# Optimization experiments

Hardware: AMD Instinct MI355X
Metric: run time of the kernel (lower is better)

## Reference

```python
import jax, jax.numpy as jnp
import numpy as np

Nh = 128
B = 4096


def _conv3d(x, w):
    # x: [B, C, D, H, W], w: [O, I, 3, 3, 3], same padding, no bias
    return jax.lax.conv_general_dilated(
        x, w, window_strides=(1, 1, 1), padding=[(1, 1)] * 3,
        dimension_numbers=("NCDHW", "OIDHW", "NCDHW"))


def setup_inputs() -> dict:
    key = jax.random.key(0)
    ks = jax.random.split(key, 12)
    x = jax.random.normal(ks[0], (B, 1024), dtype=jnp.float32)
    hidden_states = jax.random.normal(ks[1], (B, Nh, 4, 4, 4), dtype=jnp.float32)
    cw = 0.05  # small init for conv kernels
    Wz = jax.random.normal(ks[2], (Nh, Nh, 3, 3, 3), dtype=jnp.float32) * cw
    Wr = jax.random.normal(ks[3], (Nh, Nh, 3, 3, 3), dtype=jnp.float32) * cw
    Wm = jax.random.normal(ks[4], (Nh, Nh, 3, 3, 3), dtype=jnp.float32) * cw
    # biases init like np.random.rand -> uniform [0,1)
    bz = jax.random.uniform(ks[5], (1, Nh, 4, 4, 4), dtype=jnp.float32)
    br = jax.random.uniform(ks[6], (1, Nh, 4, 4, 4), dtype=jnp.float32)
    bm = jax.random.uniform(ks[7], (1, Nh, 4, 4, 4), dtype=jnp.float32)
    lw = 0.03
    Lz = jax.random.normal(ks[8], (Nh * 64, 1024), dtype=jnp.float32) * lw
    Lr = jax.random.normal(ks[9], (Nh * 64, 1024), dtype=jnp.float32) * lw
    Lm = jax.random.normal(ks[10], (Nh * 64, 1024), dtype=jnp.float32) * lw
    return dict(x=x, hidden_states=hidden_states, Wz=Wz, Wr=Wr, Wm=Wm,
                bz=bz, br=br, bm=bm, Lz=Lz, Lr=Lr, Lm=Lm)


def reference(x, hidden_states, Wz, Wr, Wm, bz, br, bm, Lz, Lr, Lm):
    # linear projections (torch Linear: x @ W.T), reshaped to voxel grid
    lz = (x @ Lz.T).reshape(B, Nh, 4, 4, 4)
    lr = (x @ Lr.T).reshape(B, Nh, 4, 4, 4)
    lm = (x @ Lm.T).reshape(B, Nh, 4, 4, 4)
    z = jax.nn.sigmoid(_conv3d(hidden_states, Wz) + lz + bz)
    r = jax.nn.sigmoid(_conv3d(hidden_states, Wr) + lr + br)
    mem = jnp.tanh(_conv3d(r * hidden_states, Wm) + lm + bm)
    return (1.0 - z) * hidden_states + z * mem
```

## Files before the change

kernel.cpp:

```cpp
#include <hip/hip_runtime.h>
#include <cstdint>

typedef __attribute__((ext_vector_type(8))) short bf16x8;
typedef __attribute__((ext_vector_type(4))) float f32x4;
typedef unsigned short u16;
typedef unsigned int u32;

static const size_t OFF_WT = 0;
static const size_t OFF_XB = 2654464;
static const size_t OFF_LB = 11043072;
static const size_t OFF_HT = 61374720;
static const size_t OFF_RH = 128483584;

__device__ __forceinline__ u16 f2bf(float x) {
  union { float f; u32 u; } v; v.f = x;
  u32 r = (v.u + 0x7FFFu + ((v.u >> 16) & 1u)) >> 16;
  return (u16)r;
}
__device__ __forceinline__ float bf2f(u16 x) {
  union { u32 u; float f; } v; v.u = ((u32)x) << 16; return v.f;
}

__device__ __forceinline__ void gload16(const void* g, void* l) {
  __builtin_amdgcn_global_load_lds(
      (const __attribute__((address_space(1))) uint32_t*)g,
      (__attribute__((address_space(3))) uint32_t*)l, 16, 0, 0);
}

__global__ __launch_bounds__(256) void k_cvt(
    const float* __restrict__ x,
    const float* __restrict__ Wz, const float* __restrict__ Wr, const float* __restrict__ Wm,
    const float* __restrict__ Lz, const float* __restrict__ Lr, const float* __restrict__ Lm,
    uint8_t* __restrict__ ws) {
  u16* wt = (u16*)(ws + OFF_WT);
  u16* xb = (u16*)(ws + OFF_XB);
  u16* lb = (u16*)(ws + OFF_LB);
  const long NWT = 3L * 27 * 128 * 128;
  const long NX  = 4096L * 1024;
  const long NL  = 3L * 8192 * 1024;
  const long total = NWT + NX + NL;
  for (long i = (long)blockIdx.x * blockDim.x + threadIdx.x; i < total;
       i += (long)gridDim.x * blockDim.x) {
    if (i < NWT) {
      long g = i / (27L * 16384);
      long r = i % (27L * 16384);
      long t = r / 16384;
      long oc = (r / 128) % 128;
      long ic = r % 128;
      const float* W = (g == 0) ? Wz : ((g == 1) ? Wr : Wm);
      wt[i] = f2bf(W[(oc * 128 + ic) * 27 + t]);
    } else if (i < NWT + NX) {
      long j = i - NWT;
      xb[j] = f2bf(x[j]);
    } else {
      long j = i - NWT - NX;
      long g = j / (8192L * 1024);
      long r = j % (8192L * 1024);
      const float* L = (g == 0) ? Lz : ((g == 1) ? Lr : Lm);
      lb[j] = f2bf(L[r]);
    }
  }
}

__global__ __launch_bounds__(256) void k_ht(const float* __restrict__ h, uint8_t* __restrict__ ws) {
  __shared__ float tile[128 * 65];
  int b = blockIdx.x;
  const float* hb = h + (size_t)b * 8192;
  u16* ht = (u16*)(ws + OFF_HT) + (size_t)b * 8192;
  for (int i = threadIdx.x; i < 8192; i += 256) {
    int ic = i >> 6, vo = i & 63;
    tile[ic * 65 + vo] = hb[i];
  }
  __syncthreads();
  for (int i = threadIdx.x; i < 8192; i += 256) {
    int vo = i >> 7, ic = i & 127;
    ht[i] = f2bf(tile[ic * 65 + vo]);
  }
}

template <int MODE>
__global__ __launch_bounds__(256) void k_conv_gemm(
    uint8_t* __restrict__ ws,
    const float* __restrict__ bz, const float* __restrict__ br, const float* __restrict__ bm,
    u32* __restrict__ dout) {
  int bx = blockIdx.x;
  int g, vo, mb;
  if (MODE == 0) { mb = bx & 31; g = (bx >> 5) & 1; vo = bx >> 6; }
  else           { mb = bx & 31; g = 2;             vo = bx >> 5; }

  const uint8_t* wt_b = ws + OFF_WT + (size_t)g * 27 * 32768;
  const uint8_t* xb_b = ws + OFF_XB;
  const uint8_t* lb_b = ws + OFF_LB + (size_t)g * 8192 * 2048;
  const uint8_t* as_b = ws + ((MODE == 0) ? OFF_HT : OFF_RH);

  __shared__ __align__(1024) uint8_t lds[65536];

  const int tid = threadIdx.x;
  const int w = tid >> 6;
  const int l = tid & 63;
  const int lrow = l >> 3;
  const int co = (((l & 7) ^ lrow) << 4);
  const int wm = (w >> 1) * 64;
  const int wn = (w & 1) * 64;
  const int lr16 = l & 15;
  const int lk = l >> 4;

  f32x4 acc[4][4];
#pragma unroll
  for (int m = 0; m < 4; ++m)
#pragma unroll
    for (int n = 0; n < 4; ++n) acc[m][n] = (f32x4){0.f, 0.f, 0.f, 0.f};

  const uint8_t* aA_x = xb_b + ((size_t)(mb * 128 + w * 32 + lrow)) * 2048 + co;
  const uint8_t* aA_t = as_b + ((size_t)(mb * 128 + w * 32 + lrow)) * 16384 + co;
  const uint8_t* aB_x = lb_b + ((size_t)(w * 32 + lrow)) * 131072 + (size_t)vo * 2048 + co;
  const uint8_t* aB_t = wt_b + ((size_t)(w * 32 + lrow)) * 256 + co;

  const int d = vo >> 4, e = (vo >> 2) & 3, f = vo & 3;
  auto validT = [&](int t) {
    int p3 = t / 9 - 1, q3 = (t / 3) % 3 - 1, s3 = t % 3 - 1;
    int dd = d + p3, ee = e + q3, ff = f + s3;
    return dd >= 0 && dd <= 3 && ee >= 0 && ee <= 3 && ff >= 0 && ff <= 3;
  };
  const int nd = 3 - (d == 0) - (d == 3);
  const int ne = 3 - (e == 0) - (e == 3);
  const int nf = 3 - (f == 0) - (f == 3);
  const int NP = 16 + 2 * nd * ne * nf;

  int s_kt = 0;
  int s_t = 0, s_ih = 0;
  while (!validT(s_t)) ++s_t;

  auto stage_next = [&](int buf) {
    uint8_t* Ad = lds + buf * 32768 + w * 4096;
    uint8_t* Bd = lds + buf * 32768 + 16384 + w * 4096;
    if (s_kt < 16) {
      int kt = s_kt;
#pragma unroll
      for (int pp = 0; pp < 4; ++pp)
        gload16(aA_x + (size_t)kt * 128 + pp * 16384, Ad + pp * 1024);
#pragma unroll
      for (int pp = 0; pp < 4; ++pp)
        gload16(aB_x + (size_t)kt * 128 + (size_t)pp * 1048576, Bd + pp * 1024);
      ++s_kt;
    } else {
      int t = s_t, ih = s_ih;
      int dd = d + t / 9 - 1, ee = e + (t / 3) % 3 - 1, ff = f + t % 3 - 1;
      int vi = dd * 16 + ee * 4 + ff;
#pragma unroll
      for (int pp = 0; pp < 4; ++pp)
        gload16(aA_t + (size_t)vi * 256 + ih * 128 + pp * 131072, Ad + pp * 1024);
#pragma unroll
      for (int pp = 0; pp < 4; ++pp)
        gload16(aB_t + (size_t)t * 32768 + ih * 128 + pp * 2048, Bd + pp * 1024);
      s_ih ^= 1;
      if (!s_ih) { do { ++s_t; } while (s_t < 27 && !validT(s_t)); }
    }
  };

  auto compute = [&](int buf) {
    const u16* At = (const u16*)(lds + buf * 32768);
    const u16* Bt = (const u16*)(lds + buf * 32768 + 16384);
#pragma unroll
    for (int ks = 0; ks < 2; ++ks) {
      bf16x8 af[4], bfr[4];
#pragma unroll
      for (int m = 0; m < 4; ++m) {
        int row = wm + m * 16 + lr16;
        int c = ks * 4 + lk;
        af[m] = *(const bf16x8*)&At[row * 64 + ((c ^ (row & 7)) * 8)];
      }
#pragma unroll
      for (int n = 0; n < 4; ++n) {
        int row = wn + n * 16 + lr16;
        int c = ks * 4 + lk;
        bfr[n] = *(const bf16x8*)&Bt[row * 64 + ((c ^ (row & 7)) * 8)];
      }
#pragma unroll
      for (int m = 0; m < 4; ++m)
#pragma unroll
        for (int n = 0; n < 4; ++n)
          acc[m][n] = __builtin_amdgcn_mfma_f32_16x16x32_bf16(af[m], bfr[n], acc[m][n], 0, 0, 0);
    }
  };

  stage_next(0);
  __syncthreads();
  for (int p = 0; p < NP; ++p) {
    int cur = p & 1;
    if (p + 1 < NP) stage_next(cur ^ 1);
    compute(cur);
    __syncthreads();
  }

  const float* bias = (MODE == 0) ? ((g == 0) ? bz : br) : bm;
  const u16* htp = (const u16*)(ws + OFF_HT);
  u16* rhp = (u16*)(ws + OFF_RH);
#pragma unroll
  for (int n = 0; n < 4; ++n) {
    int oc = wn + n * 16 + lr16;
    float bv = bias[oc * 64 + vo];
#pragma unroll
    for (int m = 0; m < 4; ++m) {
#pragma unroll
      for (int j = 0; j < 4; ++j) {
        int brow = mb * 128 + wm + m * 16 + lk * 4 + j;
        size_t pidx = (size_t)brow * 8192 + (size_t)vo * 128 + oc;
        float pre = acc[m][n][j] + bv;
        pre = fminf(fmaxf(pre, -30.f), 30.f);
        if (MODE == 0) {
          float sg = 1.f / (1.f + __expf(-pre));
          if (g == 0) {
            dout[pidx] = (u32)f2bf(sg);
          } else {
            float hv = bf2f(htp[pidx]);
            rhp[pidx] = f2bf(sg * hv);
          }
        } else {
          float e2 = __expf(-2.f * pre);
          float th = (1.f - e2) / (1.f + e2);
          u32 old = dout[pidx];
          dout[pidx] = (old & 0xFFFFu) | (((u32)f2bf(th)) << 16);
        }
      }
    }
  }
}

__global__ __launch_bounds__(256) void k_combine(const float* __restrict__ h, u32* __restrict__ dout) {
  __shared__ u32 tile[64 * 129];
  int b = blockIdx.x;
  const u32* db = dout + (size_t)b * 8192;
  for (int i = threadIdx.x; i < 8192; i += 256) {
    int vo = i >> 7, oc = i & 127;
    tile[vo * 129 + oc] = db[i];
  }
  __syncthreads();
  float* ob = (float*)dout + (size_t)b * 8192;
  const float* hb = h + (size_t)b * 8192;
  for (int o = threadIdx.x; o < 8192; o += 256) {
    int oc = o >> 6, vo = o & 63;
    u32 pk = tile[vo * 129 + oc];
    float z = bf2f((u16)(pk & 0xFFFFu));
    float mem = bf2f((u16)(pk >> 16));
    ob[o] = (1.f - z) * hb[o] + z * mem;
  }
}

extern "C" void kernel_launch(void* const* d_in, const int* in_sizes, int n_in,
                              void* d_out, int out_size, void* d_ws, size_t ws_size,
                              hipStream_t stream) {
  const float* x  = (const float*)d_in[0];
  const float* h  = (const float*)d_in[1];
  const float* Wz = (const float*)d_in[2];
  const float* Wr = (const float*)d_in[3];
  const float* Wm = (const float*)d_in[4];
  const float* bz = (const float*)d_in[5];
  const float* br = (const float*)d_in[6];
  const float* bm = (const float*)d_in[7];
  const float* Lz = (const float*)d_in[8];
  const float* Lr = (const float*)d_in[9];
  const float* Lm = (const float*)d_in[10];
  uint8_t* ws = (uint8_t*)d_ws;
  u32* dout = (u32*)d_out;

  k_cvt<<<2048, 256, 0, stream>>>(x, Wz, Wr, Wm, Lz, Lr, Lm, ws);
  k_ht<<<4096, 256, 0, stream>>>(h, ws);
  k_conv_gemm<0><<<4096, 256, 0, stream>>>(ws, bz, br, bm, dout);
  k_conv_gemm<1><<<2048, 256, 0, stream>>>(ws, bz, br, bm, dout);
  k_combine<<<4096, 256, 0, stream>>>(h, dout);
}
```

Before: 931.9 us.

## Enlarge conv-GEMM tile to 256 rows and triple-buffer LDS with vmcnt waits

The conv/linear GEMM blocks grow from 256 to 512 threads, covering 256 batch rows per block while keeping 128 output channels. This halves the grid and improves reuse of the weight (B) tiles. The double-buffered loop with a full __syncthreads per step becomes a three-stage LDS ring. It uses s_waitcnt vmcnt(6) plus a raw s_barrier, so two stages of global-to-LDS loads stay in flight while the current one is computed. The cost is 144KB of LDS per block, which allows only one block per CU and makes the hand-counted wait depend on exactly six loads per stage.

```diff
diff --git a/kernel.cpp b/kernel.cpp
--- a/kernel.cpp
+++ b/kernel.cpp
@@ -79,21 +79,21 @@
 }
 
 template <int MODE>
-__global__ __launch_bounds__(256) void k_conv_gemm(
+__global__ __launch_bounds__(512, 2) void k_conv_gemm(
     uint8_t* __restrict__ ws,
     const float* __restrict__ bz, const float* __restrict__ br, const float* __restrict__ bm,
     u32* __restrict__ dout) {
   int bx = blockIdx.x;
   int g, vo, mb;
-  if (MODE == 0) { mb = bx & 31; g = (bx >> 5) & 1; vo = bx >> 6; }
-  else           { mb = bx & 31; g = 2;             vo = bx >> 5; }
+  if (MODE == 0) { mb = bx & 15; g = (bx >> 4) & 1; vo = bx >> 5; }
+  else           { mb = bx & 15; g = 2;             vo = bx >> 4; }
 
   const uint8_t* wt_b = ws + OFF_WT + (size_t)g * 27 * 32768;
   const uint8_t* xb_b = ws + OFF_XB;
   const uint8_t* lb_b = ws + OFF_LB + (size_t)g * 8192 * 2048;
   const uint8_t* as_b = ws + ((MODE == 0) ? OFF_HT : OFF_RH);
 
-  __shared__ __align__(1024) uint8_t lds[65536];
+  __shared__ __align__(1024) uint8_t lds[3 * 49152];
 
   const int tid = threadIdx.x;
   const int w = tid >> 6;
@@ -111,10 +111,10 @@
 #pragma unroll
     for (int n = 0; n < 4; ++n) acc[m][n] = (f32x4){0.f, 0.f, 0.f, 0.f};
 
-  const uint8_t* aA_x = xb_b + ((size_t)(mb * 128 + w * 32 + lrow)) * 2048 + co;
-  const uint8_t* aA_t = as_b + ((size_t)(mb * 128 + w * 32 + lrow)) * 16384 + co;
-  const uint8_t* aB_x = lb_b + ((size_t)(w * 32 + lrow)) * 131072 + (size_t)vo * 2048 + co;
-  const uint8_t* aB_t = wt_b + ((size_t)(w * 32 + lrow)) * 256 + co;
+  const uint8_t* aA_x = xb_b + ((size_t)(mb * 256 + w * 32 + lrow)) * 2048 + co;
+  const uint8_t* aA_t = as_b + ((size_t)(mb * 256 + w * 32 + lrow)) * 16384 + co;
+  const uint8_t* aB_x = lb_b + ((size_t)(w * 16 + lrow)) * 131072 + (size_t)vo * 2048 + co;
+  const uint8_t* aB_t = wt_b + ((size_t)(w * 16 + lrow)) * 256 + co;
 
   const int d = vo >> 4, e = (vo >> 2) & 3, f = vo & 3;
   auto validT = [&](int t) {
@@ -132,35 +132,35 @@
   while (!validT(s_t)) ++s_t;
 
   auto stage_next = [&](int buf) {
-    uint8_t* Ad = lds + buf * 32768 + w * 4096;
-    uint8_t* Bd = lds + buf * 32768 + 16384 + w * 4096;
+    uint8_t* Ad = lds + buf * 49152 + w * 4096;
+    uint8_t* Bd = lds + buf * 49152 + 32768 + w * 2048;
     if (s_kt < 16) {
       int kt = s_kt;
 #pragma unroll
-      for (int pp = 0; pp < 4; ++pp)
-        gload16(aA_x + (size_t)kt * 128 + pp * 16384, Ad + pp * 1024);
-#pragma unroll
-      for (int pp = 0; pp < 4; ++pp)
-        gload16(aB_x + (size_t)kt * 128 + (size_t)pp * 1048576, Bd + pp * 1024);
+      for (int i = 0; i < 4; ++i)
+        gload16(aA_x + (size_t)kt * 128 + i * 16384, Ad + i * 1024);
+#pragma unroll
+      for (int j = 0; j < 2; ++j)
+        gload16(aB_x + (size_t)kt * 128 + (size_t)j * 1048576, Bd + j * 1024);
       ++s_kt;
     } else {
       int t = s_t, ih = s_ih;
       int dd = d + t / 9 - 1, ee = e + (t / 3) % 3 - 1, ff = f + t % 3 - 1;
       int vi = dd * 16 + ee * 4 + ff;
 #pragma unroll
-      for (int pp = 0; pp < 4; ++pp)
-        gload16(aA_t + (size_t)vi * 256 + ih * 128 + pp * 131072, Ad + pp * 1024);
-#pragma unroll
-      for (int pp = 0; pp < 4; ++pp)
-        gload16(aB_t + (size_t)t * 32768 + ih * 128 + pp * 2048, Bd + pp * 1024);
+      for (int i = 0; i < 4; ++i)
+        gload16(aA_t + (size_t)vi * 256 + ih * 128 + i * 131072, Ad + i * 1024);
+#pragma unroll
+      for (int j = 0; j < 2; ++j)
+        gload16(aB_t + (size_t)t * 32768 + ih * 128 + j * 2048, Bd + j * 1024);
       s_ih ^= 1;
       if (!s_ih) { do { ++s_t; } while (s_t < 27 && !validT(s_t)); }
     }
   };
 
   auto compute = [&](int buf) {
-    const u16* At = (const u16*)(lds + buf * 32768);
-    const u16* Bt = (const u16*)(lds + buf * 32768 + 16384);
+    const u16* At = (const u16*)(lds + buf * 49152);
+    const u16* Bt = (const u16*)(lds + buf * 49152 + 32768);
 #pragma unroll
     for (int ks = 0; ks < 2; ++ks) {
       bf16x8 af[4], bfr[4];
@@ -185,12 +185,16 @@
   };
 
   stage_next(0);
-  __syncthreads();
+  stage_next(1);
+  int cb = 0, sb = 2;
   for (int p = 0; p < NP; ++p) {
-    int cur = p & 1;
-    if (p + 1 < NP) stage_next(cur ^ 1);
-    compute(cur);
-    __syncthreads();
+    if (p + 1 < NP) asm volatile("s_waitcnt vmcnt(6)" ::: "memory");
+    else            asm volatile("s_waitcnt vmcnt(0)" ::: "memory");
+    __builtin_amdgcn_s_barrier();
+    if (p + 2 < NP) stage_next(sb);
+    compute(cb);
+    cb = (cb == 2) ? 0 : cb + 1;
+    sb = (sb == 2) ? 0 : sb + 1;
   }
 
   const float* bias = (MODE == 0) ? ((g == 0) ? bz : br) : bm;
@@ -204,7 +208,7 @@
     for (int m = 0; m < 4; ++m) {
 #pragma unroll
       for (int j = 0; j < 4; ++j) {
-        int brow = mb * 128 + wm + m * 16 + lk * 4 + j;
+        int brow = mb * 256 + wm + m * 16 + lk * 4 + j;
         size_t pidx = (size_t)brow * 8192 + (size_t)vo * 128 + oc;
         float pre = acc[m][n][j] + bv;
         pre = fminf(fmaxf(pre, -30.f), 30.f);
@@ -266,7 +270,7 @@
 
   k_cvt<<<2048, 256, 0, stream>>>(x, Wz, Wr, Wm, Lz, Lr, Lm, ws);
   k_ht<<<4096, 256, 0, stream>>>(h, ws);
-  k_conv_gemm<0><<<4096, 256, 0, stream>>>(ws, bz, br, bm, dout);
-  k_conv_gemm<1><<<2048, 256, 0, stream>>>(ws, bz, br, bm, dout);
+  k_conv_gemm<0><<<2048, 512, 0, stream>>>(ws, bz, br, bm, dout);
+  k_conv_gemm<1><<<1024, 512, 0, stream>>>(ws, bz, br, bm, dout);
   k_combine<<<4096, 256, 0, stream>>>(h, dout);
 }
```

After: 945.6 us. Within noise of the previous version (+1.5%).

## Fuse z and r gate GEMMs into one 512-thread block sharing A tiles

Applied to the files above, without the earlier changes.

The z and r gate convolution-plus-linear GEMMs now run in a single kernel. Each 512-thread block computes both gates for a 128-row batch tile, so the activation (A) tile is loaded once and used for both weight sets. Zero-padded conv taps outside the 4x4x4 grid are skipped per voxel, and block indices are remapped with an XCD-style swizzle for better L2 locality. The cost is a larger LDS footprint and more registers per block, which may limit occupancy.

```diff
diff --git a/kernel.cpp b/kernel.cpp
--- a/kernel.cpp
+++ b/kernel.cpp
@@ -78,20 +78,161 @@
   }
 }
 
-template <int MODE>
-__global__ __launch_bounds__(256) void k_conv_gemm(
+__global__ __launch_bounds__(512, 2) void k_zr_gemm(
     uint8_t* __restrict__ ws,
-    const float* __restrict__ bz, const float* __restrict__ br, const float* __restrict__ bm,
+    const float* __restrict__ bz, const float* __restrict__ br,
     u32* __restrict__ dout) {
   int bx = blockIdx.x;
-  int g, vo, mb;
-  if (MODE == 0) { mb = bx & 31; g = (bx >> 5) & 1; vo = bx >> 6; }
-  else           { mb = bx & 31; g = 2;             vo = bx >> 5; }
-
-  const uint8_t* wt_b = ws + OFF_WT + (size_t)g * 27 * 32768;
+  int L = (bx & 7) * 256 + (bx >> 3);
+  int vo = L & 63, mb = L >> 6;
+
+  const uint8_t* wt_b = ws + OFF_WT;
   const uint8_t* xb_b = ws + OFF_XB;
-  const uint8_t* lb_b = ws + OFF_LB + (size_t)g * 8192 * 2048;
-  const uint8_t* as_b = ws + ((MODE == 0) ? OFF_HT : OFF_RH);
+  const uint8_t* lb_b = ws + OFF_LB;
+  const uint8_t* ht_b = ws + OFF_HT;
+
+  __shared__ __align__(1024) uint8_t lds[2 * 49152];
+
+  const int tid = threadIdx.x;
+  const int w = tid >> 6;
+  const int l = tid & 63;
+  const int lrow = l >> 3;
+  const int co = (((l & 7) ^ lrow) << 4);
+  const int wm = (w >> 2) * 64;
+  const int wn = (w & 3) * 64;
+  const int gw = w >> 2;
+  const int lr16 = l & 15;
+  const int lk = l >> 4;
+
+  f32x4 acc[4][4];
+#pragma unroll
+  for (int m = 0; m < 4; ++m)
+#pragma unroll
+    for (int n = 0; n < 4; ++n) acc[m][n] = (f32x4){0.f, 0.f, 0.f, 0.f};
+
+  const uint8_t* aA_x = xb_b + ((size_t)(mb * 128 + w * 16 + lrow)) * 2048 + co;
+  const uint8_t* aA_t = ht_b + ((size_t)(mb * 128 + w * 16 + lrow)) * 16384 + co;
+  const uint8_t* aB_x = lb_b + (size_t)gw * 16777216 +
+                        ((size_t)((w & 3) * 32 + lrow)) * 131072 + (size_t)vo * 2048 + co;
+  const uint8_t* aB_t = wt_b + (size_t)gw * 884736 +
+                        ((size_t)((w & 3) * 32 + lrow)) * 256 + co;
+
+  const int d = vo >> 4, e = (vo >> 2) & 3, f = vo & 3;
+  auto validT = [&](int t) {
+    int p3 = t / 9 - 1, q3 = (t / 3) % 3 - 1, s3 = t % 3 - 1;
+    int dd = d + p3, ee = e + q3, ff = f + s3;
+    return dd >= 0 && dd <= 3 && ee >= 0 && ee <= 3 && ff >= 0 && ff <= 3;
+  };
+  const int nd = 3 - (d == 0) - (d == 3);
+  const int ne = 3 - (e == 0) - (e == 3);
+  const int nf = 3 - (f == 0) - (f == 3);
+  const int NP = 16 + 2 * nd * ne * nf;
+
+  int s_kt = 0;
+  int s_t = 0, s_ih = 0;
+  while (!validT(s_t)) ++s_t;
+
+  auto stage_next = [&](int buf) {
+    uint8_t* Ad = lds + buf * 49152 + w * 2048;
+    uint8_t* Bd = lds + buf * 49152 + 16384 + w * 4096;
+    if (s_kt < 16) {
+      int kt = s_kt;
+#pragma unroll
+      for (int i = 0; i < 2; ++i)
+        gload16(aA_x + (size_t)kt * 128 + (size_t)i * 16384, Ad + i * 1024);
+#pragma unroll
+      for (int j = 0; j < 4; ++j)
+        gload16(aB_x + (size_t)kt * 128 + (size_t)j * 1048576, Bd + j * 1024);
+      ++s_kt;
+    } else {
+      int t = s_t, ih = s_ih;
+      int dd = d + t / 9 - 1, ee = e + (t / 3) % 3 - 1, ff = f + t % 3 - 1;
+      int vi = dd * 16 + ee * 4 + ff;
+#pragma unroll
+      for (int i = 0; i < 2; ++i)
+        gload16(aA_t + (size_t)vi * 256 + ih * 128 + (size_t)i * 131072, Ad + i * 1024);
+#pragma unroll
+      for (int j = 0; j < 4; ++j)
+        gload16(aB_t + (size_t)t * 32768 + ih * 128 + (size_t)j * 2048, Bd + j * 1024);
+      s_ih ^= 1;
+      if (!s_ih) { do { ++s_t; } while (s_t < 27 && !validT(s_t)); }
+    }
+  };
+
+  auto compute = [&](int buf) {
+    const u16* At = (const u16*)(lds + buf * 49152);
+    const u16* Bt = (const u16*)(lds + buf * 49152 + 16384);
+#pragma unroll
+    for (int ks = 0; ks < 2; ++ks) {
+      bf16x8 af[4], bfr[4];
+#pragma unroll
+      for (int m = 0; m < 4; ++m) {
+        int row = wm + m * 16 + lr16;
+        int c = ks * 4 + lk;
+        af[m] = *(const bf16x8*)&At[row * 64 + ((c ^ (row & 7)) * 8)];
+      }
+#pragma unroll
+      for (int n = 0; n < 4; ++n) {
+        int row = wn + n * 16 + lr16;
+        int c = ks * 4 + lk;
+        bfr[n] = *(const bf16x8*)&Bt[row * 64 + ((c ^ (row & 7)) * 8)];
+      }
+#pragma unroll
+      for (int m = 0; m < 4; ++m)
+#pragma unroll
+        for (int n = 0; n < 4; ++n)
+          acc[m][n] = __builtin_amdgcn_mfma_f32_16x16x32_bf16(af[m], bfr[n], acc[m][n], 0, 0, 0);
+    }
+  };
+
+  stage_next(0);
+  __syncthreads();
+  for (int p = 0; p < NP; ++p) {
+    int cur = p & 1;
+    if (p + 1 < NP) stage_next(cur ^ 1);
+    compute(cur);
+    __syncthreads();
+  }
+
+  const int gate = wn >> 7;
+  const int ocb = wn & 127;
+  const float* bias = gate ? br : bz;
+  const u16* htp = (const u16*)(ws + OFF_HT);
+  u16* rhp = (u16*)(ws + OFF_RH);
+#pragma unroll
+  for (int n = 0; n < 4; ++n) {
+    int oc = ocb + n * 16 + lr16;
+    float bv = bias[oc * 64 + vo];
+#pragma unroll
+    for (int m = 0; m < 4; ++m) {
+#pragma unroll
+      for (int j = 0; j < 4; ++j) {
+        int brow = mb * 128 + wm + m * 16 + lk * 4 + j;
+        size_t pidx = (size_t)brow * 8192 + (size_t)vo * 128 + oc;
+        float pre = acc[m][n][j] + bv;
+        pre = fminf(fmaxf(pre, -30.f), 30.f);
+        float sg = 1.f / (1.f + __expf(-pre));
+        if (gate == 0) {
+          dout[pidx] = (u32)f2bf(sg);
+        } else {
+          float hv = bf2f(htp[pidx]);
+          rhp[pidx] = f2bf(sg * hv);
+        }
+      }
+    }
+  }
+}
+
+__global__ __launch_bounds__(256) void k_m_gemm(
+    uint8_t* __restrict__ ws, const float* __restrict__ bm, u32* __restrict__ dout) {
+  int bx = blockIdx.x;
+  int L = (bx & 7) * 256 + (bx >> 3);
+  int vo = L & 63, mb = L >> 6;
+
+  const uint8_t* wt_b = ws + OFF_WT + (size_t)2 * 27 * 32768;
+  const uint8_t* xb_b = ws + OFF_XB;
+  const uint8_t* lb_b = ws + OFF_LB + (size_t)2 * 8192 * 2048;
+  const uint8_t* as_b = ws + OFF_RH;
 
   __shared__ __align__(1024) uint8_t lds[65536];
 
@@ -193,13 +334,10 @@
     __syncthreads();
   }
 
-  const float* bias = (MODE == 0) ? ((g == 0) ? bz : br) : bm;
-  const u16* htp = (const u16*)(ws + OFF_HT);
-  u16* rhp = (u16*)(ws + OFF_RH);
 #pragma unroll
   for (int n = 0; n < 4; ++n) {
     int oc = wn + n * 16 + lr16;
-    float bv = bias[oc * 64 + vo];
+    float bv = bm[oc * 64 + vo];
 #pragma unroll
     for (int m = 0; m < 4; ++m) {
 #pragma unroll
@@ -208,20 +346,10 @@
         size_t pidx = (size_t)brow * 8192 + (size_t)vo * 128 + oc;
         float pre = acc[m][n][j] + bv;
         pre = fminf(fmaxf(pre, -30.f), 30.f);
-        if (MODE == 0) {
-          float sg = 1.f / (1.f + __expf(-pre));
-          if (g == 0) {
-            dout[pidx] = (u32)f2bf(sg);
-          } else {
-            float hv = bf2f(htp[pidx]);
-            rhp[pidx] = f2bf(sg * hv);
-          }
-        } else {
-          float e2 = __expf(-2.f * pre);
-          float th = (1.f - e2) / (1.f + e2);
-          u32 old = dout[pidx];
-          dout[pidx] = (old & 0xFFFFu) | (((u32)f2bf(th)) << 16);
-        }
+        float e2 = __expf(-2.f * pre);
+        float th = (1.f - e2) / (1.f + e2);
+        u32 old = dout[pidx];
+        dout[pidx] = (old & 0xFFFFu) | (((u32)f2bf(th)) << 16);
       }
     }
   }
@@ -266,7 +394,7 @@
 
   k_cvt<<<2048, 256, 0, stream>>>(x, Wz, Wr, Wm, Lz, Lr, Lm, ws);
   k_ht<<<4096, 256, 0, stream>>>(h, ws);
-  k_conv_gemm<0><<<4096, 256, 0, stream>>>(ws, bz, br, bm, dout);
-  k_conv_gemm<1><<<2048, 256, 0, stream>>>(ws, bz, br, bm, dout);
+  k_zr_gemm<<<2048, 512, 0, stream>>>(ws, bz, br, dout);
+  k_m_gemm<<<2048, 256, 0, stream>>>(ws, bm, dout);
   k_combine<<<4096, 256, 0, stream>>>(h, dout);
 }
```

Measured after the change: 959.5 us. +3.0%, slower.
